# Kernel tuning notes

Hardware: AMD Instinct MI355X
Metric: run time of the kernel (lower is better)

The kernel has to match this reference:

```python
import jax, jax.numpy as jnp
import numpy as np

EPS = 1.0       # epsilon
SIGMA = 1.0     # sigma
MAX_ITER = 10   # max_iter (tol=1e-6 never triggers early stop in 10 iters for random data)


def setup_inputs() -> dict:
    key = jax.random.key(0)
    k1, k2, k3, k4 = jax.random.split(key, 4)
    B, L, K, D = 8, 2048, 2048, 64
    x = jax.random.normal(k1, (B, L, D), dtype=jnp.float32)
    y = jax.random.normal(k2, (B, K, D), dtype=jnp.float32)
    a = jax.random.uniform(k3, (B, L), dtype=jnp.float32) + 1e-3
    b = jax.random.uniform(k4, (B, K), dtype=jnp.float32) + 1e-3
    a = a / jnp.sum(a, axis=1, keepdims=True)
    b = b / jnp.sum(b, axis=1, keepdims=True)
    return {"x": x, "a": a, "y": y, "b": b}


def _make_kernel(u, v):
    # energy_squared, distance_type=2: K = -clamp(||u||^2 + ||v||^2 - 2 u.v, 0) / sigma^2
    outer = jnp.einsum('bld,bkd->blk', u, v)
    nu = jnp.sum(u * u, axis=2)
    nv = jnp.sum(v * v, axis=2)
    dist = jnp.maximum(nu[:, :, None] + nv[:, None, :] - 2.0 * outer, 0.0) / (SIGMA ** 2)
    return -dist


def _extrap(pot, logw, kern):
    # -eps * logsumexp((K + pot[:,None,:]) / eps + logw[:,None,:], axis=2)
    return -EPS * jax.scipy.special.logsumexp(
        (kern + pot[:, None, :]) / EPS + logw[:, None, :], axis=2)


def reference(x, a, y, b):
    sg = jax.lax.stop_gradient
    Kxx = _make_kernel(x, x)
    Kyy = _make_kernel(y, y)
    Kxy = _make_kernel(x, y)
    Kyx = _make_kernel(y, x)
    la = jnp.log(a)
    lb = jnp.log(b)

    # Sinkhorn fixed-point loop runs under no_grad in the original ('loop' surgery)
    sKxx, sKyy, sKxy, sKyx = sg(Kxx), sg(Kyy), sg(Kxy), sg(Kyx)
    sla, slb = sg(la), sg(lb)

    def body(i, state):
        pxx, pyy, pxy, pyx = state
        nxx = _extrap(pxx, sla, sKxx)  # dir 'xx', rev 'xx'
        nyy = _extrap(pyy, slb, sKyy)  # dir 'yy', rev 'yy'
        nxy = _extrap(pyx, slb, sKxy)  # dir 'xy', rev 'yx'
        nyx = _extrap(pxy, sla, sKyx)  # dir 'yx', rev 'xy'
        return ((nxx + pxx) * 0.5, (nyy + pyy) * 0.5,
                (nxy + pxy) * 0.5, (nyx + pyx) * 0.5)

    init = (jnp.zeros_like(la), jnp.zeros_like(lb),
            jnp.zeros_like(la), jnp.zeros_like(lb))
    pxx, pyy, pxy, pyx = jax.lax.fori_loop(0, MAX_ITER, body, init)
    pxx, pyy, pxy, pyx = sg(pxx), sg(pyy), sg(pxy), sg(pyx)

    # Final differentiable extrapolation (rho=None -> potential_transform is identity)
    f = _extrap(pxx, la, Kxx)   # (B, L)
    fe = _extrap(pxy, la, Kyx)  # (B, K)
    g = _extrap(pyy, lb, Kyy)   # (B, K)
    ge = _extrap(pyx, lb, Kxy)  # (B, L)

    diff_r = jnp.where(a == 0, 0.0, ge - f)
    diff_l = jnp.where(b == 0, 0.0, fe - g)
    res = jnp.sum(diff_r * a, axis=1) + jnp.sum(diff_l * b, axis=1)
    return jnp.mean(res)
```

## Files before the change

kernel.cpp:

```cpp
#include <hip/hip_runtime.h>
#include <stdint.h>

#define BATCH 8
#define NPTS  2048
#define DIM   64
#define VECN  (BATCH*NPTS)
#define CHUNK 64
#define NCHUNK (NPTS/CHUNK)

typedef __attribute__((ext_vector_type(8))) short bf16x8;
typedef __attribute__((ext_vector_type(4))) float f32x4;

#define IL2 1.4426950408889634f
#define LN2 0.6931471805599453f

__device__ inline float fexp2(float x) { return __builtin_amdgcn_exp2f(x); }
__device__ inline float flog2(float x) { return __builtin_amdgcn_logf(x); }

__device__ inline void gload_lds16(const void* g, void* l) {
  __builtin_amdgcn_global_load_lds(
      (const __attribute__((address_space(1))) uint32_t*)g,
      (__attribute__((address_space(3))) uint32_t*)l, 16, 0, 0);
}
__device__ inline void gload_lds4(const void* g, void* l) {
  __builtin_amdgcn_global_load_lds(
      (const __attribute__((address_space(1))) uint32_t*)g,
      (__attribute__((address_space(3))) uint32_t*)l, 4, 0, 0);
}

static constexpr size_t XB_OFF   = 0;
static constexpr size_t YB_OFF   = (size_t)VECN * DIM * 2;
static constexpr size_t NX2_OFF  = YB_OFF * 2;
static constexpr size_t NY2_OFF  = NX2_OFF + (size_t)VECN * 4;
static constexpr size_t LA2_OFF  = NY2_OFF + (size_t)VECN * 4;
static constexpr size_t LB2_OFF  = LA2_OFF + (size_t)VECN * 4;
static constexpr size_t POT_OFF  = LB2_OFF + (size_t)VECN * 4;
static constexpr size_t NW0_OFF  = POT_OFF + (size_t)4 * VECN * 4;
static constexpr size_t NW1_OFF  = NW0_OFF + (size_t)4 * VECN * 8;
static constexpr size_t FOUT_OFF = NW1_OFF + (size_t)4 * VECN * 8;
static constexpr size_t R_OFF    = FOUT_OFF + (size_t)4 * VECN * 4;

__device__ inline ushort f2bf(float f) {
  uint32_t u = __float_as_uint(f);
  u += 0x7fffu + ((u >> 16) & 1u);
  return (ushort)(u >> 16);
}

__global__ void prep_convert(const float* __restrict__ x, const float* __restrict__ y,
                             ushort* __restrict__ xb, ushort* __restrict__ yb,
                             float* __restrict__ nx2, float* __restrict__ ny2) {
  int wid  = (blockIdx.x * blockDim.x + threadIdx.x) >> 6;
  int lane = threadIdx.x & 63;
  const float* src; ushort* dst; float* nrm; int row;
  if (wid < VECN) { src = x; dst = xb; nrm = nx2; row = wid; }
  else            { src = y; dst = yb; nrm = ny2; row = wid - VECN; }
  float v = src[(size_t)row * DIM + lane];
  dst[(size_t)row * DIM + lane] = f2bf(v);
  float sq = v * v;
  #pragma unroll
  for (int off = 32; off; off >>= 1) sq += __shfl_xor(sq, off);
  if (lane == 0) nrm[row] = sq * IL2;
}

__global__ void prep_vecs(const float* __restrict__ a, const float* __restrict__ b,
                          const float* __restrict__ nx2, const float* __restrict__ ny2,
                          float* __restrict__ la2, float* __restrict__ lb2,
                          float* __restrict__ pot,
                          float2* __restrict__ nw0, float2* __restrict__ nw1) {
  int i = blockIdx.x * blockDim.x + threadIdx.x;
  float l2a = log2f(a[i]);
  float l2b = log2f(b[i]);
  la2[i] = l2a;
  lb2[i] = l2b;
  float nxv = nx2[i], nyv = ny2[i];
  float2 vx = make_float2(nxv, l2a), vy = make_float2(nyv, l2b);
  nw0[i]                    = vx;  nw1[i]                    = vx;
  nw0[(size_t)VECN + i]     = vy;  nw1[(size_t)VECN + i]     = vy;
  nw0[(size_t)2*VECN + i]   = vy;  nw1[(size_t)2*VECN + i]   = vy;
  nw0[(size_t)3*VECN + i]   = vx;  nw1[(size_t)3*VECN + i]   = vx;
  #pragma unroll
  for (int j = 0; j < 4; ++j) pot[(size_t)j * VECN + i] = 0.f;
}

__global__ __launch_bounds__(256, 8)
void extrap_online(const ushort* __restrict__ xb, const ushort* __restrict__ yb,
                   const float* __restrict__ nx2, const float* __restrict__ ny2,
                   const float2* __restrict__ nwin, float2* __restrict__ nwout,
                   const float* __restrict__ la2, const float* __restrict__ lb2,
                   float* __restrict__ pot, float* __restrict__ Rarr,
                   float* __restrict__ fouts, int avg) {
  __shared__ char vlds[2][CHUNK * 128];
  __shared__ char nwlds[2][CHUNK * 8];

  const int rb    = blockIdx.x;
  const int batch = blockIdx.y;
  const int z     = blockIdx.z;
  const ushort *U, *V; const float *nU2;
  switch (z) {
    case 0:  U = xb; V = xb; nU2 = nx2; break;
    case 1:  U = yb; V = yb; nU2 = ny2; break;
    case 2:  U = xb; V = yb; nU2 = nx2; break;
    default: U = yb; V = xb; nU2 = ny2; break;
  }
  const int lane = threadIdx.x & 63;
  const int w    = threadIdx.x >> 6;
  const int g    = lane >> 4;
  const int c    = lane & 15;
  const int rowbase = rb * 64 + w * 16;

  const ushort* Ub  = U + ((size_t)batch * NPTS + rowbase) * DIM;
  const char*   Vch = (const char*)(V + (size_t)batch * NPTS * DIM);
  const char*   nwch = (const char*)(nwin + (size_t)z * VECN + (size_t)batch * NPTS);

  bf16x8 a0 = *(const bf16x8*)(Ub + (size_t)c * DIM + g * 8);
  bf16x8 a1 = *(const bf16x8*)(Ub + (size_t)c * DIM + 32 + g * 8);

  float nxr2[4];
  #pragma unroll
  for (int r = 0; r < 4; ++r) nxr2[r] = nU2[(size_t)batch * NPTS + rowbase + g * 4 + r];

  const size_t lane_voff = ((size_t)(lane >> 3)) * 128
                         + (size_t)((((lane & 7) ^ (lane >> 3)) << 4));

  float m[4], s[4];
  #pragma unroll
  for (int r = 0; r < 4; ++r) { m[r] = -INFINITY; s[r] = 0.f; }

  auto stage = [&](int p, int ck) {
    const char* gbase = Vch + (size_t)ck * CHUNK * 128;
    #pragma unroll
    for (int i = 0; i < 2; ++i) {
      int j = w * 2 + i;
      gload_lds16(gbase + (size_t)j * 1024 + lane_voff, &vlds[p][j * 1024]);
    }
    if (w == 0) {
      const char* gn = nwch + (size_t)ck * CHUNK * 8;
      gload_lds4(gn + lane * 4,       &nwlds[p][0]);
      gload_lds4(gn + 256 + lane * 4, &nwlds[p][256]);
    }
  };

  auto compute = [&](int p) {
    #pragma unroll
    for (int t = 0; t < 2; ++t) {
      const int rr0 = t * 32 + c;
      const int rr1 = rr0 + 16;
      const int x0 = (rr0 & 7) << 4;
      const char* pv0 = &vlds[p][rr0 * 128];
      const char* pv1 = &vlds[p][rr1 * 128];
      bf16x8 b0a = *(const bf16x8*)(pv0 + ((g * 16) ^ x0));
      bf16x8 b0b = *(const bf16x8*)(pv0 + ((64 + g * 16) ^ x0));
      bf16x8 b1a = *(const bf16x8*)(pv1 + ((g * 16) ^ x0));
      bf16x8 b1b = *(const bf16x8*)(pv1 + ((64 + g * 16) ^ x0));
      float2 nw0 = *(const float2*)&nwlds[p][rr0 * 8];
      float2 nw1 = *(const float2*)&nwlds[p][rr1 * 8];

      f32x4 acc0 = {0.f, 0.f, 0.f, 0.f}, acc1 = {0.f, 0.f, 0.f, 0.f};
      acc0 = __builtin_amdgcn_mfma_f32_16x16x32_bf16(a0, b0a, acc0, 0, 0, 0);
      acc0 = __builtin_amdgcn_mfma_f32_16x16x32_bf16(a1, b0b, acc0, 0, 0, 0);
      acc1 = __builtin_amdgcn_mfma_f32_16x16x32_bf16(a0, b1a, acc1, 0, 0, 0);
      acc1 = __builtin_amdgcn_mfma_f32_16x16x32_bf16(a1, b1b, acc1, 0, 0, 0);

      #pragma unroll
      for (int r = 0; r < 4; ++r) {
        float d0 = fmaxf(fmaf(-2.f * IL2, acc0[r], nxr2[r] + nw0.x), 0.f);
        float d1 = fmaxf(fmaf(-2.f * IL2, acc1[r], nxr2[r] + nw1.x), 0.f);
        float t0 = nw0.y - d0;
        float t1 = nw1.y - d1;
        float mn = fmaxf(m[r], fmaxf(t0, t1));
        s[r] = fmaf(s[r], fexp2(m[r] - mn), fexp2(t0 - mn) + fexp2(t1 - mn));
        m[r] = mn;
      }
    }
  };

  stage(0, 0);
  __syncthreads();
  int p = 0;
  for (int ck = 0; ck < NCHUNK; ++ck) {
    if (ck < NCHUNK - 1) stage(p ^ 1, ck + 1);
    compute(p);
    __syncthreads();
    p ^= 1;
  }

  #pragma unroll
  for (int r = 0; r < 4; ++r) {
    #pragma unroll
    for (int off = 1; off < 16; off <<= 1) {
      float mo = __shfl_xor(m[r], off);
      float so = __shfl_xor(s[r], off);
      float mn = fmaxf(m[r], mo);
      s[r] = fmaf(s[r], fexp2(m[r] - mn), so * fexp2(mo - mn));
      m[r] = mn;
    }
  }
  if (c == 0) {
    const int cjob = z ^ (z >> 1);
    const float* lw2 = (z & 1) ? lb2 : la2;
    #pragma unroll
    for (int r = 0; r < 4; ++r) {
      int rowi = batch * NPTS + rowbase + g * 4 + r;
      size_t pi = (size_t)z * VECN + rowi;
      float lse = m[r] + flog2(fmaxf(s[r], 1e-38f));
      float val = -LN2 * lse;
      if (avg) {
        val = 0.5f * (val + pot[pi]);
        pot[pi] = val;
        Rarr[pi] = lse;
        nwout[(size_t)cjob * VECN + rowi].y = fmaf(val, IL2, lw2[rowi]);
      } else {
        fouts[pi] = val;
      }
    }
  }
}

__global__ __launch_bounds__(256, 8)
void extrap_fixed(const ushort* __restrict__ xb, const ushort* __restrict__ yb,
                  const float* __restrict__ nx2, const float* __restrict__ ny2,
                  const float2* __restrict__ nwin, float2* __restrict__ nwout,
                  const float* __restrict__ la2, const float* __restrict__ lb2,
                  float* __restrict__ pot, float* __restrict__ Rarr,
                  float* __restrict__ fouts, int avg) {
  __shared__ char vlds[2][CHUNK * 128];
  __shared__ char nwlds[2][CHUNK * 8];

  const int rb    = blockIdx.x;
  const int batch = blockIdx.y;
  const int z     = blockIdx.z;
  const ushort *U, *V; const float *nU2;
  switch (z) {
    case 0:  U = xb; V = xb; nU2 = nx2; break;
    case 1:  U = yb; V = yb; nU2 = ny2; break;
    case 2:  U = xb; V = yb; nU2 = nx2; break;
    default: U = yb; V = xb; nU2 = ny2; break;
  }
  const int lane = threadIdx.x & 63;
  const int w    = threadIdx.x >> 6;
  const int g    = lane >> 4;
  const int c    = lane & 15;
  const int rowbase = rb * 64 + w * 16;

  const ushort* Ub  = U + ((size_t)batch * NPTS + rowbase) * DIM;
  const char*   Vch = (const char*)(V + (size_t)batch * NPTS * DIM);
  const char*   nwch = (const char*)(nwin + (size_t)z * VECN + (size_t)batch * NPTS);

  bf16x8 a0 = *(const bf16x8*)(Ub + (size_t)c * DIM + g * 8);
  bf16x8 a1 = *(const bf16x8*)(Ub + (size_t)c * DIM + 32 + g * 8);

  float q[4], Rr[4];
  #pragma unroll
  for (int r = 0; r < 4; ++r) {
    size_t rowi = (size_t)batch * NPTS + rowbase + g * 4 + r;
    Rr[r] = Rarr[(size_t)z * VECN + rowi];
    q[r]  = -(nU2[rowi] + Rr[r]);
  }

  const size_t lane_voff = ((size_t)(lane >> 3)) * 128
                         + (size_t)((((lane & 7) ^ (lane >> 3)) << 4));

  float s[4] = {0.f, 0.f, 0.f, 0.f};

  auto stage = [&](int p, int ck) {
    const char* gbase = Vch + (size_t)ck * CHUNK * 128;
    #pragma unroll
    for (int i = 0; i < 2; ++i) {
      int j = w * 2 + i;
      gload_lds16(gbase + (size_t)j * 1024 + lane_voff, &vlds[p][j * 1024]);
    }
    if (w == 0) {
      const char* gn = nwch + (size_t)ck * CHUNK * 8;
      gload_lds4(gn + lane * 4,       &nwlds[p][0]);
      gload_lds4(gn + 256 + lane * 4, &nwlds[p][256]);
    }
  };

  auto compute = [&](int p) {
    #pragma unroll
    for (int t = 0; t < 2; ++t) {
      const int rr0 = t * 32 + c;
      const int rr1 = rr0 + 16;
      const int x0 = (rr0 & 7) << 4;
      const char* pv0 = &vlds[p][rr0 * 128];
      const char* pv1 = &vlds[p][rr1 * 128];
      bf16x8 b0a = *(const bf16x8*)(pv0 + ((g * 16) ^ x0));
      bf16x8 b0b = *(const bf16x8*)(pv0 + ((64 + g * 16) ^ x0));
      bf16x8 b1a = *(const bf16x8*)(pv1 + ((g * 16) ^ x0));
      bf16x8 b1b = *(const bf16x8*)(pv1 + ((64 + g * 16) ^ x0));
      float2 nw0 = *(const float2*)&nwlds[p][rr0 * 8];
      float2 nw1 = *(const float2*)&nwlds[p][rr1 * 8];
      float ct0 = nw0.y - nw0.x;
      float ct1 = nw1.y - nw1.x;

      f32x4 acc0 = {0.f, 0.f, 0.f, 0.f}, acc1 = {0.f, 0.f, 0.f, 0.f};
      acc0 = __builtin_amdgcn_mfma_f32_16x16x32_bf16(a0, b0a, acc0, 0, 0, 0);
      acc0 = __builtin_amdgcn_mfma_f32_16x16x32_bf16(a1, b0b, acc0, 0, 0, 0);
      acc1 = __builtin_amdgcn_mfma_f32_16x16x32_bf16(a0, b1a, acc1, 0, 0, 0);
      acc1 = __builtin_amdgcn_mfma_f32_16x16x32_bf16(a1, b1b, acc1, 0, 0, 0);

      #pragma unroll
      for (int r = 0; r < 4; ++r) {
        s[r] += fexp2(fmaf(2.f * IL2, acc0[r], ct0 + q[r]));
        s[r] += fexp2(fmaf(2.f * IL2, acc1[r], ct1 + q[r]));
      }
    }
  };

  stage(0, 0);
  __syncthreads();
  int p = 0;
  for (int ck = 0; ck < NCHUNK; ++ck) {
    if (ck < NCHUNK - 1) stage(p ^ 1, ck + 1);
    compute(p);
    __syncthreads();
    p ^= 1;
  }

  #pragma unroll
  for (int r = 0; r < 4; ++r) {
    #pragma unroll
    for (int off = 1; off < 16; off <<= 1) s[r] += __shfl_xor(s[r], off);
  }
  if (c == 0) {
    const int cjob = z ^ (z >> 1);
    const float* lw2 = (z & 1) ? lb2 : la2;
    #pragma unroll
    for (int r = 0; r < 4; ++r) {
      int rowi = batch * NPTS + rowbase + g * 4 + r;
      size_t pi = (size_t)z * VECN + rowi;
      float lse = Rr[r] + flog2(fmaxf(s[r], 1e-38f));
      float val = -LN2 * lse;
      if (avg) {
        val = 0.5f * (val + pot[pi]);
        pot[pi] = val;
        Rarr[pi] = lse;
        nwout[(size_t)cjob * VECN + rowi].y = fmaf(val, IL2, lw2[rowi]);
      } else {
        fouts[pi] = val;
      }
    }
  }
}

__global__ void reduce_kernel(const float* __restrict__ fouts,
                              const float* __restrict__ a, const float* __restrict__ b,
                              float* __restrict__ out) {
  const float* f  = fouts;
  const float* g  = fouts + (size_t)VECN;
  const float* ge = fouts + (size_t)2 * VECN;
  const float* fe = fouts + (size_t)3 * VECN;
  int tid = threadIdx.x;
  float acc = 0.f;
  for (int i = tid; i < VECN; i += 1024)
    acc += (ge[i] - f[i]) * a[i] + (fe[i] - g[i]) * b[i];
  #pragma unroll
  for (int off = 32; off; off >>= 1) acc += __shfl_xor(acc, off);
  __shared__ float red[16];
  if ((tid & 63) == 0) red[tid >> 6] = acc;
  __syncthreads();
  if (tid < 64) {
    float v = (tid < 16) ? red[tid] : 0.f;
    #pragma unroll
    for (int off = 8; off; off >>= 1) v += __shfl_xor(v, off);
    if (tid == 0) out[0] = v / (float)BATCH;
  }
}

extern "C" void kernel_launch(void* const* d_in, const int* in_sizes, int n_in,
                              void* d_out, int out_size, void* d_ws, size_t ws_size,
                              hipStream_t stream) {
  const float* x = (const float*)d_in[0];
  const float* a = (const float*)d_in[1];
  const float* y = (const float*)d_in[2];
  const float* b = (const float*)d_in[3];
  char* ws = (char*)d_ws;
  ushort* xb  = (ushort*)(ws + XB_OFF);
  ushort* yb  = (ushort*)(ws + YB_OFF);
  float* nx2  = (float*)(ws + NX2_OFF);
  float* ny2  = (float*)(ws + NY2_OFF);
  float* la2  = (float*)(ws + LA2_OFF);
  float* lb2  = (float*)(ws + LB2_OFF);
  float* pot  = (float*)(ws + POT_OFF);
  float2* nw0 = (float2*)(ws + NW0_OFF);
  float2* nw1 = (float2*)(ws + NW1_OFF);
  float* fouts= (float*)(ws + FOUT_OFF);
  float* Rarr = (float*)(ws + R_OFF);

  prep_convert<<<dim3(2 * VECN / 4), 256, 0, stream>>>(x, y, xb, yb, nx2, ny2);
  prep_vecs<<<dim3(VECN / 256), 256, 0, stream>>>(a, b, nx2, ny2, la2, lb2, pot, nw0, nw1);

  const dim3 eg(NPTS / 64, BATCH, 4);
  float2* bufs[2] = {nw0, nw1};
  extrap_online<<<eg, 256, 0, stream>>>(xb, yb, nx2, ny2, bufs[0], bufs[1],
                                        la2, lb2, pot, Rarr, fouts, 1);
  for (int it = 1; it < 10; ++it) {
    extrap_fixed<<<eg, 256, 0, stream>>>(xb, yb, nx2, ny2,
                                         bufs[it & 1], bufs[(it & 1) ^ 1],
                                         la2, lb2, pot, Rarr, fouts, 1);
  }
  extrap_fixed<<<eg, 256, 0, stream>>>(xb, yb, nx2, ny2,
                                       bufs[10 & 1], bufs[(10 & 1) ^ 1],
                                       la2, lb2, pot, Rarr, fouts, 0);

  reduce_kernel<<<1, 1024, 0, stream>>>(fouts, a, b, (float*)d_out);
}
```

Before: 505.6 us.

## Pair jobs sharing the same V matrix per block and enlarge staged chunks

Each block now processes two extrapolation jobs that share the same column operand (xx with yx, yy with xy), so every staged V tile in LDS feeds two sets of MFMAs and exp reductions. This halves the grid's z dimension and halves the global and LDS traffic for V. Chunk size grows from 64 to 256 rows, giving fewer barriers and larger 16-byte loads for the weight vectors, while launch bounds drop to 2 blocks per CU. The cost is more registers and LDS per block, lower occupancy, and a grid half the previous size (512 blocks), which may leave the GPU underfilled.

```diff
diff --git a/kernel.cpp b/kernel.cpp
--- a/kernel.cpp
+++ b/kernel.cpp
@@ -5,7 +5,7 @@
 #define NPTS  2048
 #define DIM   64
 #define VECN  (BATCH*NPTS)
-#define CHUNK 64
+#define CHUNK 256
 #define NCHUNK (NPTS/CHUNK)
 
 typedef __attribute__((ext_vector_type(8))) short bf16x8;
@@ -21,11 +21,6 @@
   __builtin_amdgcn_global_load_lds(
       (const __attribute__((address_space(1))) uint32_t*)g,
       (__attribute__((address_space(3))) uint32_t*)l, 16, 0, 0);
-}
-__device__ inline void gload_lds4(const void* g, void* l) {
-  __builtin_amdgcn_global_load_lds(
-      (const __attribute__((address_space(1))) uint32_t*)g,
-      (__attribute__((address_space(3))) uint32_t*)l, 4, 0, 0);
 }
 
 static constexpr size_t XB_OFF   = 0;
@@ -82,7 +77,8 @@
   for (int j = 0; j < 4; ++j) pot[(size_t)j * VECN + i] = 0.f;
 }
 
-__global__ __launch_bounds__(256, 8)
+
+__global__ __launch_bounds__(256, 2)
 void extrap_online(const ushort* __restrict__ xb, const ushort* __restrict__ yb,
                    const float* __restrict__ nx2, const float* __restrict__ ny2,
                    const float2* __restrict__ nwin, float2* __restrict__ nwout,
@@ -90,59 +86,75 @@
                    float* __restrict__ pot, float* __restrict__ Rarr,
                    float* __restrict__ fouts, int avg) {
   __shared__ char vlds[2][CHUNK * 128];
-  __shared__ char nwlds[2][CHUNK * 8];
+  __shared__ char nwlds[2][2][CHUNK * 8];
 
   const int rb    = blockIdx.x;
   const int batch = blockIdx.y;
-  const int z     = blockIdx.z;
-  const ushort *U, *V; const float *nU2;
-  switch (z) {
-    case 0:  U = xb; V = xb; nU2 = nx2; break;
-    case 1:  U = yb; V = yb; nU2 = ny2; break;
-    case 2:  U = xb; V = yb; nU2 = nx2; break;
-    default: U = yb; V = xb; nU2 = ny2; break;
-  }
+  const int pair  = blockIdx.z;
+  const int zA = pair ? 1 : 0, zB = pair ? 2 : 3;
+  const ushort* V  = pair ? yb : xb;
+  const ushort* UA = pair ? yb : xb;
+  const ushort* UB = pair ? xb : yb;
+  const float* nUA = pair ? ny2 : nx2;
+  const float* nUB = pair ? nx2 : ny2;
+
   const int lane = threadIdx.x & 63;
   const int w    = threadIdx.x >> 6;
   const int g    = lane >> 4;
   const int c    = lane & 15;
   const int rowbase = rb * 64 + w * 16;
 
-  const ushort* Ub  = U + ((size_t)batch * NPTS + rowbase) * DIM;
+  const ushort* UbA = UA + ((size_t)batch * NPTS + rowbase) * DIM;
+  const ushort* UbB = UB + ((size_t)batch * NPTS + rowbase) * DIM;
   const char*   Vch = (const char*)(V + (size_t)batch * NPTS * DIM);
-  const char*   nwch = (const char*)(nwin + (size_t)z * VECN + (size_t)batch * NPTS);
-
-  bf16x8 a0 = *(const bf16x8*)(Ub + (size_t)c * DIM + g * 8);
-  bf16x8 a1 = *(const bf16x8*)(Ub + (size_t)c * DIM + 32 + g * 8);
-
-  float nxr2[4];
-  #pragma unroll
-  for (int r = 0; r < 4; ++r) nxr2[r] = nU2[(size_t)batch * NPTS + rowbase + g * 4 + r];
+  const char*   nwchA = (const char*)(nwin + (size_t)zA * VECN + (size_t)batch * NPTS);
+  const char*   nwchB = (const char*)(nwin + (size_t)zB * VECN + (size_t)batch * NPTS);
+
+  bf16x8 aA0 = *(const bf16x8*)(UbA + (size_t)c * DIM + g * 8);
+  bf16x8 aA1 = *(const bf16x8*)(UbA + (size_t)c * DIM + 32 + g * 8);
+  bf16x8 aB0 = *(const bf16x8*)(UbB + (size_t)c * DIM + g * 8);
+  bf16x8 aB1 = *(const bf16x8*)(UbB + (size_t)c * DIM + 32 + g * 8);
+
+  float nxA[4], nxB[4];
+  #pragma unroll
+  for (int r = 0; r < 4; ++r) {
+    size_t rowi = (size_t)batch * NPTS + rowbase + g * 4 + r;
+    nxA[r] = nUA[rowi];
+    nxB[r] = nUB[rowi];
+  }
 
   const size_t lane_voff = ((size_t)(lane >> 3)) * 128
                          + (size_t)((((lane & 7) ^ (lane >> 3)) << 4));
 
-  float m[4], s[4];
-  #pragma unroll
-  for (int r = 0; r < 4; ++r) { m[r] = -INFINITY; s[r] = 0.f; }
+  float mA[4], sA[4], mB[4], sB[4];
+  #pragma unroll
+  for (int r = 0; r < 4; ++r) {
+    mA[r] = -INFINITY; sA[r] = 0.f;
+    mB[r] = -INFINITY; sB[r] = 0.f;
+  }
 
   auto stage = [&](int p, int ck) {
     const char* gbase = Vch + (size_t)ck * CHUNK * 128;
     #pragma unroll
-    for (int i = 0; i < 2; ++i) {
-      int j = w * 2 + i;
+    for (int i = 0; i < 8; ++i) {
+      int j = w * 8 + i;
       gload_lds16(gbase + (size_t)j * 1024 + lane_voff, &vlds[p][j * 1024]);
     }
     if (w == 0) {
-      const char* gn = nwch + (size_t)ck * CHUNK * 8;
-      gload_lds4(gn + lane * 4,       &nwlds[p][0]);
-      gload_lds4(gn + 256 + lane * 4, &nwlds[p][256]);
+      const char* gn = nwchA + (size_t)ck * CHUNK * 8;
+      gload_lds16(gn + lane * 16,        &nwlds[p][0][0]);
+      gload_lds16(gn + 1024 + lane * 16, &nwlds[p][0][1024]);
+    }
+    if (w == 1) {
+      const char* gn = nwchB + (size_t)ck * CHUNK * 8;
+      gload_lds16(gn + lane * 16,        &nwlds[p][1][0]);
+      gload_lds16(gn + 1024 + lane * 16, &nwlds[p][1][1024]);
     }
   };
 
   auto compute = [&](int p) {
     #pragma unroll
-    for (int t = 0; t < 2; ++t) {
+    for (int t = 0; t < 8; ++t) {
       const int rr0 = t * 32 + c;
       const int rr1 = rr0 + 16;
       const int x0 = (rr0 & 7) << 4;
@@ -152,24 +164,44 @@
       bf16x8 b0b = *(const bf16x8*)(pv0 + ((64 + g * 16) ^ x0));
       bf16x8 b1a = *(const bf16x8*)(pv1 + ((g * 16) ^ x0));
       bf16x8 b1b = *(const bf16x8*)(pv1 + ((64 + g * 16) ^ x0));
-      float2 nw0 = *(const float2*)&nwlds[p][rr0 * 8];
-      float2 nw1 = *(const float2*)&nwlds[p][rr1 * 8];
-
-      f32x4 acc0 = {0.f, 0.f, 0.f, 0.f}, acc1 = {0.f, 0.f, 0.f, 0.f};
-      acc0 = __builtin_amdgcn_mfma_f32_16x16x32_bf16(a0, b0a, acc0, 0, 0, 0);
-      acc0 = __builtin_amdgcn_mfma_f32_16x16x32_bf16(a1, b0b, acc0, 0, 0, 0);
-      acc1 = __builtin_amdgcn_mfma_f32_16x16x32_bf16(a0, b1a, acc1, 0, 0, 0);
-      acc1 = __builtin_amdgcn_mfma_f32_16x16x32_bf16(a1, b1b, acc1, 0, 0, 0);
-
-      #pragma unroll
-      for (int r = 0; r < 4; ++r) {
-        float d0 = fmaxf(fmaf(-2.f * IL2, acc0[r], nxr2[r] + nw0.x), 0.f);
-        float d1 = fmaxf(fmaf(-2.f * IL2, acc1[r], nxr2[r] + nw1.x), 0.f);
-        float t0 = nw0.y - d0;
-        float t1 = nw1.y - d1;
-        float mn = fmaxf(m[r], fmaxf(t0, t1));
-        s[r] = fmaf(s[r], fexp2(m[r] - mn), fexp2(t0 - mn) + fexp2(t1 - mn));
-        m[r] = mn;
+      float2 nwA0 = *(const float2*)&nwlds[p][0][rr0 * 8];
+      float2 nwA1 = *(const float2*)&nwlds[p][0][rr1 * 8];
+      float2 nwB0 = *(const float2*)&nwlds[p][1][rr0 * 8];
+      float2 nwB1 = *(const float2*)&nwlds[p][1][rr1 * 8];
+
+      {
+        f32x4 acc0 = {0.f, 0.f, 0.f, 0.f}, acc1 = {0.f, 0.f, 0.f, 0.f};
+        acc0 = __builtin_amdgcn_mfma_f32_16x16x32_bf16(aA0, b0a, acc0, 0, 0, 0);
+        acc0 = __builtin_amdgcn_mfma_f32_16x16x32_bf16(aA1, b0b, acc0, 0, 0, 0);
+        acc1 = __builtin_amdgcn_mfma_f32_16x16x32_bf16(aA0, b1a, acc1, 0, 0, 0);
+        acc1 = __builtin_amdgcn_mfma_f32_16x16x32_bf16(aA1, b1b, acc1, 0, 0, 0);
+        #pragma unroll
+        for (int r = 0; r < 4; ++r) {
+          float d0 = fmaxf(fmaf(-2.f * IL2, acc0[r], nxA[r] + nwA0.x), 0.f);
+          float d1 = fmaxf(fmaf(-2.f * IL2, acc1[r], nxA[r] + nwA1.x), 0.f);
+          float t0 = nwA0.y - d0;
+          float t1 = nwA1.y - d1;
+          float mn = fmaxf(mA[r], fmaxf(t0, t1));
+          sA[r] = fmaf(sA[r], fexp2(mA[r] - mn), fexp2(t0 - mn) + fexp2(t1 - mn));
+          mA[r] = mn;
+        }
+      }
+      {
+        f32x4 acc0 = {0.f, 0.f, 0.f, 0.f}, acc1 = {0.f, 0.f, 0.f, 0.f};
+        acc0 = __builtin_amdgcn_mfma_f32_16x16x32_bf16(aB0, b0a, acc0, 0, 0, 0);
+        acc0 = __builtin_amdgcn_mfma_f32_16x16x32_bf16(aB1, b0b, acc0, 0, 0, 0);
+        acc1 = __builtin_amdgcn_mfma_f32_16x16x32_bf16(aB0, b1a, acc1, 0, 0, 0);
+        acc1 = __builtin_amdgcn_mfma_f32_16x16x32_bf16(aB1, b1b, acc1, 0, 0, 0);
+        #pragma unroll
+        for (int r = 0; r < 4; ++r) {
+          float d0 = fmaxf(fmaf(-2.f * IL2, acc0[r], nxB[r] + nwB0.x), 0.f);
+          float d1 = fmaxf(fmaf(-2.f * IL2, acc1[r], nxB[r] + nwB1.x), 0.f);
+          float t0 = nwB0.y - d0;
+          float t1 = nwB1.y - d1;
+          float mn = fmaxf(mB[r], fmaxf(t0, t1));
+          sB[r] = fmaf(sB[r], fexp2(mB[r] - mn), fexp2(t0 - mn) + fexp2(t1 - mn));
+          mB[r] = mn;
+        }
       }
     }
   };
@@ -188,35 +220,50 @@
   for (int r = 0; r < 4; ++r) {
     #pragma unroll
     for (int off = 1; off < 16; off <<= 1) {
-      float mo = __shfl_xor(m[r], off);
-      float so = __shfl_xor(s[r], off);
-      float mn = fmaxf(m[r], mo);
-      s[r] = fmaf(s[r], fexp2(m[r] - mn), so * fexp2(mo - mn));
-      m[r] = mn;
+      float mo = __shfl_xor(mA[r], off);
+      float so = __shfl_xor(sA[r], off);
+      float mn = fmaxf(mA[r], mo);
+      sA[r] = fmaf(sA[r], fexp2(mA[r] - mn), so * fexp2(mo - mn));
+      mA[r] = mn;
+      mo = __shfl_xor(mB[r], off);
+      so = __shfl_xor(sB[r], off);
+      mn = fmaxf(mB[r], mo);
+      sB[r] = fmaf(sB[r], fexp2(mB[r] - mn), so * fexp2(mo - mn));
+      mB[r] = mn;
     }
   }
   if (c == 0) {
-    const int cjob = z ^ (z >> 1);
-    const float* lw2 = (z & 1) ? lb2 : la2;
+    const int cjobA = zA ^ (zA >> 1);
+    const int cjobB = zB ^ (zB >> 1);
+    const float* lwA = (zA & 1) ? lb2 : la2;
+    const float* lwB = (zB & 1) ? lb2 : la2;
     #pragma unroll
     for (int r = 0; r < 4; ++r) {
       int rowi = batch * NPTS + rowbase + g * 4 + r;
-      size_t pi = (size_t)z * VECN + rowi;
-      float lse = m[r] + flog2(fmaxf(s[r], 1e-38f));
-      float val = -LN2 * lse;
+      size_t piA = (size_t)zA * VECN + rowi;
+      size_t piB = (size_t)zB * VECN + rowi;
+      float lseA = mA[r] + flog2(fmaxf(sA[r], 1e-38f));
+      float lseB = mB[r] + flog2(fmaxf(sB[r], 1e-38f));
+      float valA = -LN2 * lseA;
+      float valB = -LN2 * lseB;
       if (avg) {
-        val = 0.5f * (val + pot[pi]);
-        pot[pi] = val;
-        Rarr[pi] = lse;
-        nwout[(size_t)cjob * VECN + rowi].y = fmaf(val, IL2, lw2[rowi]);
+        valA = 0.5f * (valA + pot[piA]);
+        pot[piA] = valA;
+        Rarr[piA] = lseA;
+        nwout[(size_t)cjobA * VECN + rowi].y = fmaf(valA, IL2, lwA[rowi]);
+        valB = 0.5f * (valB + pot[piB]);
+        pot[piB] = valB;
+        Rarr[piB] = lseB;
+        nwout[(size_t)cjobB * VECN + rowi].y = fmaf(valB, IL2, lwB[rowi]);
       } else {
-        fouts[pi] = val;
-      }
-    }
-  }
-}
-
-__global__ __launch_bounds__(256, 8)
+        fouts[piA] = valA;
+        fouts[piB] = valB;
+      }
+    }
+  }
+}
+
+__global__ __launch_bounds__(256, 2)
 void extrap_fixed(const ushort* __restrict__ xb, const ushort* __restrict__ yb,
                   const float* __restrict__ nx2, const float* __restrict__ ny2,
                   const float2* __restrict__ nwin, float2* __restrict__ nwout,
@@ -224,61 +271,73 @@
                   float* __restrict__ pot, float* __restrict__ Rarr,
                   float* __restrict__ fouts, int avg) {
   __shared__ char vlds[2][CHUNK * 128];
-  __shared__ char nwlds[2][CHUNK * 8];
+  __shared__ char nwlds[2][2][CHUNK * 8];
 
   const int rb    = blockIdx.x;
   const int batch = blockIdx.y;
-  const int z     = blockIdx.z;
-  const ushort *U, *V; const float *nU2;
-  switch (z) {
-    case 0:  U = xb; V = xb; nU2 = nx2; break;
-    case 1:  U = yb; V = yb; nU2 = ny2; break;
-    case 2:  U = xb; V = yb; nU2 = nx2; break;
-    default: U = yb; V = xb; nU2 = ny2; break;
-  }
+  const int pair  = blockIdx.z;
+  const int zA = pair ? 1 : 0, zB = pair ? 2 : 3;
+  const ushort* V  = pair ? yb : xb;
+  const ushort* UA = pair ? yb : xb;
+  const ushort* UB = pair ? xb : yb;
+  const float* nUA = pair ? ny2 : nx2;
+  const float* nUB = pair ? nx2 : ny2;
+
   const int lane = threadIdx.x & 63;
   const int w    = threadIdx.x >> 6;
   const int g    = lane >> 4;
   const int c    = lane & 15;
   const int rowbase = rb * 64 + w * 16;
 
-  const ushort* Ub  = U + ((size_t)batch * NPTS + rowbase) * DIM;
+  const ushort* UbA = UA + ((size_t)batch * NPTS + rowbase) * DIM;
+  const ushort* UbB = UB + ((size_t)batch * NPTS + rowbase) * DIM;
   const char*   Vch = (const char*)(V + (size_t)batch * NPTS * DIM);
-  const char*   nwch = (const char*)(nwin + (size_t)z * VECN + (size_t)batch * NPTS);
-
-  bf16x8 a0 = *(const bf16x8*)(Ub + (size_t)c * DIM + g * 8);
-  bf16x8 a1 = *(const bf16x8*)(Ub + (size_t)c * DIM + 32 + g * 8);
-
-  float q[4], Rr[4];
+  const char*   nwchA = (const char*)(nwin + (size_t)zA * VECN + (size_t)batch * NPTS);
+  const char*   nwchB = (const char*)(nwin + (size_t)zB * VECN + (size_t)batch * NPTS);
+
+  bf16x8 aA0 = *(const bf16x8*)(UbA + (size_t)c * DIM + g * 8);
+  bf16x8 aA1 = *(const bf16x8*)(UbA + (size_t)c * DIM + 32 + g * 8);
+  bf16x8 aB0 = *(const bf16x8*)(UbB + (size_t)c * DIM + g * 8);
+  bf16x8 aB1 = *(const bf16x8*)(UbB + (size_t)c * DIM + 32 + g * 8);
+
+  float qA[4], RrA[4], qB[4], RrB[4];
   #pragma unroll
   for (int r = 0; r < 4; ++r) {
     size_t rowi = (size_t)batch * NPTS + rowbase + g * 4 + r;
-    Rr[r] = Rarr[(size_t)z * VECN + rowi];
-    q[r]  = -(nU2[rowi] + Rr[r]);
+    RrA[r] = Rarr[(size_t)zA * VECN + rowi];
+    qA[r]  = -(nUA[rowi] + RrA[r]);
+    RrB[r] = Rarr[(size_t)zB * VECN + rowi];
+    qB[r]  = -(nUB[rowi] + RrB[r]);
   }
 
   const size_t lane_voff = ((size_t)(lane >> 3)) * 128
                          + (size_t)((((lane & 7) ^ (lane >> 3)) << 4));
 
-  float s[4] = {0.f, 0.f, 0.f, 0.f};
+  float sA[4] = {0.f, 0.f, 0.f, 0.f};
+  float sB[4] = {0.f, 0.f, 0.f, 0.f};
 
   auto stage = [&](int p, int ck) {
     const char* gbase = Vch + (size_t)ck * CHUNK * 128;
     #pragma unroll
-    for (int i = 0; i < 2; ++i) {
-      int j = w * 2 + i;
+    for (int i = 0; i < 8; ++i) {
+      int j = w * 8 + i;
       gload_lds16(gbase + (size_t)j * 1024 + lane_voff, &vlds[p][j * 1024]);
     }
     if (w == 0) {
-      const char* gn = nwch + (size_t)ck * CHUNK * 8;
-      gload_lds4(gn + lane * 4,       &nwlds[p][0]);
-      gload_lds4(gn + 256 + lane * 4, &nwlds[p][256]);
+      const char* gn = nwchA + (size_t)ck * CHUNK * 8;
+      gload_lds16(gn + lane * 16,        &nwlds[p][0][0]);
+      gload_lds16(gn + 1024 + lane * 16, &nwlds[p][0][1024]);
+    }
+    if (w == 1) {
+      const char* gn = nwchB + (size_t)ck * CHUNK * 8;
+      gload_lds16(gn + lane * 16,        &nwlds[p][1][0]);
+      gload_lds16(gn + 1024 + lane * 16, &nwlds[p][1][1024]);
     }
   };
 
   auto compute = [&](int p) {
     #pragma unroll
-    for (int t = 0; t < 2; ++t) {
+    for (int t = 0; t < 8; ++t) {
       const int rr0 = t * 32 + c;
       const int rr1 = rr0 + 16;
       const int x0 = (rr0 & 7) << 4;
@@ -288,21 +347,36 @@
       bf16x8 b0b = *(const bf16x8*)(pv0 + ((64 + g * 16) ^ x0));
       bf16x8 b1a = *(const bf16x8*)(pv1 + ((g * 16) ^ x0));
       bf16x8 b1b = *(const bf16x8*)(pv1 + ((64 + g * 16) ^ x0));
-      float2 nw0 = *(const float2*)&nwlds[p][rr0 * 8];
-      float2 nw1 = *(const float2*)&nwlds[p][rr1 * 8];
-      float ct0 = nw0.y - nw0.x;
-      float ct1 = nw1.y - nw1.x;
-
-      f32x4 acc0 = {0.f, 0.f, 0.f, 0.f}, acc1 = {0.f, 0.f, 0.f, 0.f};
-      acc0 = __builtin_amdgcn_mfma_f32_16x16x32_bf16(a0, b0a, acc0, 0, 0, 0);
-      acc0 = __builtin_amdgcn_mfma_f32_16x16x32_bf16(a1, b0b, acc0, 0, 0, 0);
-      acc1 = __builtin_amdgcn_mfma_f32_16x16x32_bf16(a0, b1a, acc1, 0, 0, 0);
-      acc1 = __builtin_amdgcn_mfma_f32_16x16x32_bf16(a1, b1b, acc1, 0, 0, 0);
-
-      #pragma unroll
-      for (int r = 0; r < 4; ++r) {
-        s[r] += fexp2(fmaf(2.f * IL2, acc0[r], ct0 + q[r]));
-        s[r] += fexp2(fmaf(2.f * IL2, acc1[r], ct1 + q[r]));
+      float2 nwA0 = *(const float2*)&nwlds[p][0][rr0 * 8];
+      float2 nwA1 = *(const float2*)&nwlds[p][0][rr1 * 8];
+      float2 nwB0 = *(const float2*)&nwlds[p][1][rr0 * 8];
+      float2 nwB1 = *(const float2*)&nwlds[p][1][rr1 * 8];
+      float ctA0 = nwA0.y - nwA0.x, ctA1 = nwA1.y - nwA1.x;
+      float ctB0 = nwB0.y - nwB0.x, ctB1 = nwB1.y - nwB1.x;
+
+      {
+        f32x4 acc0 = {0.f, 0.f, 0.f, 0.f}, acc1 = {0.f, 0.f, 0.f, 0.f};
+        acc0 = __builtin_amdgcn_mfma_f32_16x16x32_bf16(aA0, b0a, acc0, 0, 0, 0);
+        acc0 = __builtin_amdgcn_mfma_f32_16x16x32_bf16(aA1, b0b, acc0, 0, 0, 0);
+        acc1 = __builtin_amdgcn_mfma_f32_16x16x32_bf16(aA0, b1a, acc1, 0, 0, 0);
+        acc1 = __builtin_amdgcn_mfma_f32_16x16x32_bf16(aA1, b1b, acc1, 0, 0, 0);
+        #pragma unroll
+        for (int r = 0; r < 4; ++r) {
+          sA[r] += fexp2(fmaf(2.f * IL2, acc0[r], ctA0 + qA[r]));
+          sA[r] += fexp2(fmaf(2.f * IL2, acc1[r], ctA1 + qA[r]));
+        }
+      }
+      {
+        f32x4 acc0 = {0.f, 0.f, 0.f, 0.f}, acc1 = {0.f, 0.f, 0.f, 0.f};
+        acc0 = __builtin_amdgcn_mfma_f32_16x16x32_bf16(aB0, b0a, acc0, 0, 0, 0);
+        acc0 = __builtin_amdgcn_mfma_f32_16x16x32_bf16(aB1, b0b, acc0, 0, 0, 0);
+        acc1 = __builtin_amdgcn_mfma_f32_16x16x32_bf16(aB0, b1a, acc1, 0, 0, 0);
+        acc1 = __builtin_amdgcn_mfma_f32_16x16x32_bf16(aB1, b1b, acc1, 0, 0, 0);
+        #pragma unroll
+        for (int r = 0; r < 4; ++r) {
+          sB[r] += fexp2(fmaf(2.f * IL2, acc0[r], ctB0 + qB[r]));
+          sB[r] += fexp2(fmaf(2.f * IL2, acc1[r], ctB1 + qB[r]));
+        }
       }
     }
   };
@@ -320,24 +394,37 @@
   #pragma unroll
   for (int r = 0; r < 4; ++r) {
     #pragma unroll
-    for (int off = 1; off < 16; off <<= 1) s[r] += __shfl_xor(s[r], off);
+    for (int off = 1; off < 16; off <<= 1) {
+      sA[r] += __shfl_xor(sA[r], off);
+      sB[r] += __shfl_xor(sB[r], off);
+    }
   }
   if (c == 0) {
-    const int cjob = z ^ (z >> 1);
-    const float* lw2 = (z & 1) ? lb2 : la2;
+    const int cjobA = zA ^ (zA >> 1);
+    const int cjobB = zB ^ (zB >> 1);
+    const float* lwA = (zA & 1) ? lb2 : la2;
+    const float* lwB = (zB & 1) ? lb2 : la2;
     #pragma unroll
     for (int r = 0; r < 4; ++r) {
       int rowi = batch * NPTS + rowbase + g * 4 + r;
-      size_t pi = (size_t)z * VECN + rowi;
-      float lse = Rr[r] + flog2(fmaxf(s[r], 1e-38f));
-      float val = -LN2 * lse;
+      size_t piA = (size_t)zA * VECN + rowi;
+      size_t piB = (size_t)zB * VECN + rowi;
+      float lseA = RrA[r] + flog2(fmaxf(sA[r], 1e-38f));
+      float lseB = RrB[r] + flog2(fmaxf(sB[r], 1e-38f));
+      float valA = -LN2 * lseA;
+      float valB = -LN2 * lseB;
       if (avg) {
-        val = 0.5f * (val + pot[pi]);
-        pot[pi] = val;
-        Rarr[pi] = lse;
-        nwout[(size_t)cjob * VECN + rowi].y = fmaf(val, IL2, lw2[rowi]);
+        valA = 0.5f * (valA + pot[piA]);
+        pot[piA] = valA;
+        Rarr[piA] = lseA;
+        nwout[(size_t)cjobA * VECN + rowi].y = fmaf(valA, IL2, lwA[rowi]);
+        valB = 0.5f * (valB + pot[piB]);
+        pot[piB] = valB;
+        Rarr[piB] = lseB;
+        nwout[(size_t)cjobB * VECN + rowi].y = fmaf(valB, IL2, lwB[rowi]);
       } else {
-        fouts[pi] = val;
+        fouts[piA] = valA;
+        fouts[piB] = valB;
       }
     }
   }
@@ -390,7 +477,7 @@
   prep_convert<<<dim3(2 * VECN / 4), 256, 0, stream>>>(x, y, xb, yb, nx2, ny2);
   prep_vecs<<<dim3(VECN / 256), 256, 0, stream>>>(a, b, nx2, ny2, la2, lb2, pot, nw0, nw1);
 
-  const dim3 eg(NPTS / 64, BATCH, 4);
+  const dim3 eg(NPTS / 64, BATCH, 2);
   float2* bufs[2] = {nw0, nw1};
   extrap_online<<<eg, 256, 0, stream>>>(xb, yb, nx2, ny2, bufs[0], bufs[1],
                                         la2, lb2, pot, Rarr, fouts, 1);
```

Result: faster. 478.8 us (-5.3%).
